# Optimization experiments

Hardware: AMD Instinct MI355X
Metric: run time of the kernel (lower is better)

The kernel has to match this reference:

```python
import jax, jax.numpy as jnp
import numpy as np
import math

B, S, H = 2, 2048, 4096
N_HEADS, HEAD_DIM = 32, 128
ROPE_THETA = 10000.0


def _rope_tables(seq_len, head_dim, dtype):
    inv_freq = 1.0 / (ROPE_THETA ** (jnp.arange(0, head_dim, 2, dtype=jnp.float32) / head_dim))
    t = jnp.arange(seq_len, dtype=jnp.float32)
    freqs = jnp.outer(t, inv_freq)                    # [S, D/2]
    emb = jnp.concatenate([freqs, freqs], axis=-1)    # [S, D]
    return jnp.cos(emb).astype(dtype), jnp.sin(emb).astype(dtype)


def _rotate_half(x):
    d = x.shape[-1] // 2
    return jnp.concatenate([-x[..., d:], x[..., :d]], axis=-1)


def setup_inputs() -> dict:
    key = jax.random.key(0)
    k0, k1, k2, k3, k4 = jax.random.split(key, 5)
    hidden_states = jax.random.normal(k0, (B, S, H), dtype=jnp.float32)
    # additive causal mask: 0 on/below diagonal, -1e9 above
    causal = jnp.triu(jnp.full((S, S), -1e9, dtype=jnp.float32), k=1)
    attention_mask = jnp.broadcast_to(causal, (B, 1, S, S))
    # BitNet b1.58 ternary weights {-1,0,1} with per-layer scalar scale
    wq = jax.random.randint(k1, (H, H), -1, 2).astype(jnp.float32)
    wk = jax.random.randint(k2, (H, H), -1, 2).astype(jnp.float32)
    wv = jax.random.randint(k3, (H, H), -1, 2).astype(jnp.float32)
    wo = jax.random.randint(k4, (H, H), -1, 2).astype(jnp.float32)
    scale = jnp.float32(0.02)
    return {"hidden_states": hidden_states, "attention_mask": attention_mask,
            "wq": wq, "wk": wk, "wv": wv, "wo": wo,
            "sq": scale, "sk": scale, "sv": scale, "so": scale}


def reference(hidden_states, attention_mask, wq, wk, wv, wo, sq, sk, sv, so):
    bsz, q_len, _ = hidden_states.shape
    dtype = hidden_states.dtype

    def qlin(x, w, s):  # QuantizedLinear: x @ (w_ternary * scale)^T
        return jnp.einsum('bsh,oh->bso', x, w) * s

    def split_heads(x):  # [B,S,H] -> [B,nH,S,D]
        return x.reshape(bsz, q_len, N_HEADS, HEAD_DIM).transpose(0, 2, 1, 3)

    q = split_heads(qlin(hidden_states, wq, sq))
    k = split_heads(qlin(hidden_states, wk, sk))
    v = split_heads(qlin(hidden_states, wv, sv))

    cos, sin = _rope_tables(q_len, HEAD_DIM, dtype)   # [S, D]
    q = q * cos + _rotate_half(q) * sin
    k = k * cos + _rotate_half(k) * sin

    scores = jnp.einsum('bnqd,bnkd->bnqk', q, k) / math.sqrt(HEAD_DIM)
    scores = scores + attention_mask
    scores = jnp.maximum(scores, jnp.finfo(scores.dtype).min)
    attn = jax.nn.softmax(scores, axis=-1)
    out = jnp.einsum('bnqk,bnkd->bnqd', attn, v)       # [B,nH,S,D]
    out = out.transpose(0, 2, 1, 3).reshape(bsz, q_len, N_HEADS * HEAD_DIM)
    return jnp.einsum('bsh,oh->bso', out, wo) * so
```

## Files before the change

### kernel.cpp

```cpp
#include <hip/hip_runtime.h>
#include <stdint.h>
#include <math.h>


#define HDIM   4096
#define SEQ    2048
#define NBATCH 2
#define NROWS  (NBATCH * SEQ)
#define NHEADS 32
#define DHEAD  128
#define QBLK   128

typedef __attribute__((ext_vector_type(8))) short short8;
typedef __attribute__((ext_vector_type(4))) short short4v;
typedef __attribute__((ext_vector_type(4))) float f32x4;
typedef unsigned short u16;
typedef unsigned int   u32;

__device__ __forceinline__ float bf2f(u16 u) {
  union { float f; u32 i; } x; x.i = ((u32)u) << 16; return x.f;
}
__device__ __forceinline__ u16 f2bf(float f) {
  union { float f; u32 i; } x; x.f = f;
  u32 r = x.i + 0x7FFFu + ((x.i >> 16) & 1u);
  return (u16)(r >> 16);
}
__device__ __forceinline__ u16 f2bf_t(float f) {
  union { float f; u32 i; } x; x.f = f;
  return (u16)(x.i >> 16);
}
__device__ __forceinline__ float exp2v(float x) {
  float r; asm("v_exp_f32 %0, %1" : "=v"(r) : "v"(x)); return r;
}

__device__ __forceinline__ void gload16(const u16* g, u16* l) {
  __builtin_amdgcn_global_load_lds(
      (const __attribute__((address_space(1))) u32*)g,
      (__attribute__((address_space(3))) u32*)l, 16, 0, 0);
}

__device__ __forceinline__ void unpack2(u32 v, float& a, float& b) {
  a = bf2f((u16)(v & 0xffffu)); b = bf2f((u16)(v >> 16));
}
__device__ __forceinline__ u32 pack2(float a, float b) {
  return (u32)f2bf(a) | ((u32)f2bf(b) << 16);
}

__global__ void f2bf_vec(const float* __restrict__ in, u16* __restrict__ out, int n4) {
  int i = blockIdx.x * blockDim.x + threadIdx.x;
  const int stride = gridDim.x * blockDim.x;
  for (; i < n4; i += stride) {
    float4 v = reinterpret_cast<const float4*>(in)[i];
    u32 lo = (u32)f2bf(v.x) | ((u32)f2bf(v.y) << 16);
    u32 hi = (u32)f2bf(v.z) | ((u32)f2bf(v.w) << 16);
    reinterpret_cast<uint2*>(out)[i] = make_uint2(lo, hi);
  }
}

__global__ void rope_tables_k(float* __restrict__ cosT, float* __restrict__ sinT) {
  int idx = blockIdx.x * blockDim.x + threadIdx.x;
  if (idx >= SEQ * 64) return;
  int s = idx >> 6, d = idx & 63;
  float ex = (float)(2 * d) / 128.0f;
  float inv = powf(10000.0f, -ex);
  float f = (float)s * inv;
  cosT[idx] = cosf(f);
  sinT[idx] = sinf(f);
}

template<int OUTF>
__global__ __launch_bounds__(512, 2)
void gemm8(const u16* __restrict__ Am, const u16* __restrict__ Bm,
           void* __restrict__ Cout, const float* __restrict__ scale_ptr,
           const float* __restrict__ cosT, const float* __restrict__ sinT) {
  extern __shared__ __align__(16) u16 ldsp[];

  const int tid = threadIdx.x;
  const int w = tid >> 6, lane = tid & 63;
  const int llo = lane & 15, lhi = (lane >> 4) & 3;
  const int wr = w >> 2, wc = w & 3;

  const int bid = blockIdx.x;
  const int xcd = bid & 7, ii = bid >> 3;
  const int by = (xcd >> 1) * 4 + (ii & 3);
  const int bx = (xcd & 1) * 8 + (ii >> 2);
  const int rowBase = by * 256, colBase = bx * 256;
  const float scl = scale_ptr[0];

  auto stage_half = [&](const u16* G, int obase, int ts, int h, int opB) {
    const int p = ts & 1;
    const u32 base = (opB ? 32768u : 0u) + (u32)p * 16384u + (u32)h * 8192u;
#pragma unroll
    for (int i = 0; i < 2; ++i) {
      const int ru = i * 64 + w * 8;
      const int r = ru + (lane >> 3);
      const int cc = (lane & 7) ^ (r & 7);
      gload16(G + (size_t)(obase + h * 128 + r) * HDIM + ts * 64 + cc * 8,
              ldsp + base + (u32)ru * 64u);
    }
  };

  f32x4 acc[8][4];
#pragma unroll
  for (int m = 0; m < 8; ++m)
#pragma unroll
    for (int n = 0; n < 4; ++n) acc[m][n] = (f32x4)0.0f;

#define PH(TCUR, MH, NH, TS, H, OPB, DOSTAGE, VMN) do {                          \
    const int p_ = (TCUR) & 1;                                                   \
    short8 af_[4][2]; short8 bf_[2][2];                                          \
    const u32 ab_ = (u32)(p_ * 16384 + (MH) * 8192);                             \
    const u32 bb_ = (u32)(32768 + p_ * 16384 + (NH) * 8192);                     \
    _Pragma("unroll")                                                            \
    for (int m4 = 0; m4 < 4; ++m4) { const int r_ = wr * 64 + m4 * 16 + llo;     \
      _Pragma("unroll")                                                          \
      for (int kk = 0; kk < 2; ++kk) { const int c_ = kk * 4 + lhi;              \
        af_[m4][kk] = *reinterpret_cast<const short8*>(                          \
            ldsp + ab_ + r_ * 64 + ((c_ ^ (r_ & 7)) * 8)); } }                   \
    _Pragma("unroll")                                                            \
    for (int n2 = 0; n2 < 2; ++n2) { const int r_ = wc * 32 + n2 * 16 + llo;     \
      _Pragma("unroll")                                                          \
      for (int kk = 0; kk < 2; ++kk) { const int c_ = kk * 4 + lhi;              \
        bf_[n2][kk] = *reinterpret_cast<const short8*>(                          \
            ldsp + bb_ + r_ * 64 + ((c_ ^ (r_ & 7)) * 8)); } }                   \
    if (DOSTAGE) stage_half((OPB) ? Bm : Am, (OPB) ? colBase : rowBase,          \
                            (TS), (H), (OPB));                                   \
    __builtin_amdgcn_s_barrier();                                                \
    asm volatile("s_waitcnt lgkmcnt(0)" ::: "memory");                           \
    __builtin_amdgcn_s_setprio(1);                                               \
    _Pragma("unroll")                                                            \
    for (int m4 = 0; m4 < 4; ++m4)                                               \
      _Pragma("unroll")                                                          \
      for (int n2 = 0; n2 < 2; ++n2)                                             \
        _Pragma("unroll")                                                        \
        for (int kk = 0; kk < 2; ++kk)                                           \
          acc[(MH) * 4 + m4][(NH) * 2 + n2] =                                    \
              __builtin_amdgcn_mfma_f32_16x16x32_bf16(                           \
                  af_[m4][kk], bf_[n2][kk],                                      \
                  acc[(MH) * 4 + m4][(NH) * 2 + n2], 0, 0, 0);                   \
    __builtin_amdgcn_s_setprio(0);                                               \
    if ((VMN) == 4) asm volatile("s_waitcnt vmcnt(4)" ::: "memory");             \
    if ((VMN) == 0) asm volatile("s_waitcnt vmcnt(0)" ::: "memory");             \
    __builtin_amdgcn_s_barrier();                                                \
  } while (0)

  stage_half(Am, rowBase, 0, 0, 0);
  stage_half(Bm, colBase, 0, 0, 1);
  stage_half(Am, rowBase, 0, 1, 0);
  stage_half(Bm, colBase, 0, 1, 1);
  stage_half(Am, rowBase, 1, 0, 0);
  stage_half(Bm, colBase, 1, 0, 1);
  asm volatile("s_waitcnt vmcnt(4)" ::: "memory");
  __builtin_amdgcn_s_barrier();

  for (int it = 0; it < 31; ++it) {
    const int T = 2 * it;
    PH(T,     0, 0, T + 1, 1, 0, 1, -1);
    PH(T,     0, 1, T + 1, 1, 1, 1, -1);
    PH(T,     1, 0, T + 2, 0, 0, 1, -1);
    PH(T,     1, 1, T + 2, 0, 1, 1,  4);
    PH(T + 1, 0, 0, T + 2, 1, 0, 1, -1);
    PH(T + 1, 0, 1, T + 2, 1, 1, 1, -1);
    PH(T + 1, 1, 0, T + 3, 0, 0, 1, -1);
    PH(T + 1, 1, 1, T + 3, 0, 1, 1,  4);
  }
  PH(62, 0, 0, 63, 1, 0, 1, -1);
  PH(62, 0, 1, 63, 1, 1, 1, -1);
  PH(62, 1, 0,  0, 0, 0, 0, -1);
  PH(62, 1, 1,  0, 0, 0, 0,  0);
  PH(63, 0, 0,  0, 0, 0, 0, -1);
  PH(63, 0, 1,  0, 0, 0, 0, -1);
  PH(63, 1, 0,  0, 0, 0, 0, -1);
  PH(63, 1, 1,  0, 0, 0, 0, -1);
#undef PH

  if (OUTF == 1) {
    float* ldf = reinterpret_cast<float*>(ldsp);
    float* Cf = reinterpret_cast<float*>(Cout);
#pragma unroll
    for (int hh = 0; hh < 2; ++hh) {
      if (hh) __syncthreads();
#pragma unroll
      for (int mf2 = 0; mf2 < 4; ++mf2)
#pragma unroll
        for (int nf = 0; nf < 4; ++nf)
#pragma unroll
          for (int r = 0; r < 4; ++r) {
            const int mf = hh * 4 + mf2;
            const int rowL = wr * 64 + mf2 * 16 + lhi * 4 + r;
            const int col = (nf >> 1) * 128 + wc * 32 + (nf & 1) * 16 + llo;
            ldf[rowL * 256 + col] = acc[mf][nf][r] * scl;
          }
      __syncthreads();
#pragma unroll
      for (int k = 0; k < 16; ++k) {
        const int rowL = k * 8 + w;
        const float4 v = *reinterpret_cast<const float4*>(&ldf[rowL * 256 + lane * 4]);
        *reinterpret_cast<float4*>(
            &Cf[(size_t)(rowBase + hh * 128 + rowL) * HDIM + colBase + lane * 4]) = v;
      }
    }
  } else {
#pragma unroll
    for (int mf = 0; mf < 8; ++mf)
#pragma unroll
      for (int nf = 0; nf < 4; ++nf)
#pragma unroll
        for (int r = 0; r < 4; ++r) {
          const int row = (mf >> 2) * 128 + wr * 64 + (mf & 3) * 16 + lhi * 4 + r;
          const int col = (nf >> 1) * 128 + wc * 32 + (nf & 1) * 16 + llo;
          ldsp[row * 256 + col] = f2bf(acc[mf][nf][r] * scl);
        }
    __syncthreads();
    u16* Cb = reinterpret_cast<u16*>(Cout);
#pragma unroll
    for (int k = 0; k < 16; ++k) {
      const int row = k * 16 + w * 2 + (lane >> 5);
      const int ch = lane & 31;
      if (OUTF == 2) {
        const int R = rowBase + row;
        const int pos = R & (SEQ - 1);
        const int cb = ch * 8;
        const int dl = cb & 63;
        const bool lohalf = (cb & 64) == 0;
        const short8 xv = *reinterpret_cast<const short8*>(&ldsp[row * 256 + cb]);
        const short8 pv = *reinterpret_cast<const short8*>(&ldsp[row * 256 + (cb ^ 64)]);
        const float* cT = &cosT[pos * 64 + dl];
        const float* sT = &sinT[pos * 64 + dl];
        u32 wds[4];
#pragma unroll
        for (int jj = 0; jj < 4; ++jj) {
          const float c0 = cT[jj * 2], c1 = cT[jj * 2 + 1];
          const float s0 = sT[jj * 2], s1 = sT[jj * 2 + 1];
          const float x0 = bf2f((u16)xv[jj * 2]), x1 = bf2f((u16)xv[jj * 2 + 1]);
          const float p0 = bf2f((u16)pv[jj * 2]), p1 = bf2f((u16)pv[jj * 2 + 1]);
          const float o0 = lohalf ? (x0 * c0 - p0 * s0) : (x0 * c0 + p0 * s0);
          const float o1 = lohalf ? (x1 * c1 - p1 * s1) : (x1 * c1 + p1 * s1);
          wds[jj] = pack2(o0, o1);
        }
        uint4 ov = make_uint4(wds[0], wds[1], wds[2], wds[3]);
        *reinterpret_cast<uint4*>(&Cb[(size_t)R * HDIM + colBase + cb]) = ov;
      } else {
        const short8 v = *reinterpret_cast<const short8*>(&ldsp[row * 256 + ch * 8]);
        *reinterpret_cast<short8*>(&Cb[(size_t)(rowBase + row) * HDIM + colBase + ch * 8]) = v;
      }
    }
  }
}

__global__ __launch_bounds__(512, 4)
void attn_causal(const u16* __restrict__ Q, const u16* __restrict__ K,
                 const u16* __restrict__ VT, u16* __restrict__ O) {
  __shared__ __align__(16) u16 Ks[2][64][128];
  __shared__ __align__(16) u16 Vt[128][72];
  __shared__ __align__(16) u16 Pw[8][16][76];

  const int tid = threadIdx.x;
  const int w = tid >> 6, lane = tid & 63;
  const int lhi = lane >> 4, llo = lane & 15;
  const int bh = blockIdx.y, b = bh >> 5, h = bh & 31;

  const u16* Kg = K + ((size_t)b * SEQ) * HDIM + h * DHEAD;
  const u16* VTg = VT + (size_t)(h * DHEAD) * NROWS + b * SEQ;

  const int kcp = tid & 15;
  const int vd = tid >> 2, vko = tid & 3;

  const float smul2 = 0.127517427f;
  int buf = 0;

  for (int halfq = 0; halfq < 2; ++halfq) {
    const int xq = (halfq == 0) ? (int)blockIdx.x : 15 - (int)blockIdx.x;
    const int qb = xq * QBLK;
    const int ntile = qb / 64 + 2;
    const int wmax = qb + w * 16 + 15;

    const u16* Qg = Q + ((size_t)(b * SEQ + qb)) * HDIM + h * DHEAD;
    short8 qf[4];
#pragma unroll
    for (int dc = 0; dc < 4; ++dc)
      qf[dc] = *reinterpret_cast<const short8*>(Qg + (size_t)(w * 16 + llo) * HDIM + dc * 32 + lhi * 8);

    f32x4 o[8];
#pragma unroll
    for (int dt = 0; dt < 8; ++dt) o[dt] = (f32x4)0.0f;
    float mrow[4], lrow[4];
#pragma unroll
    for (int r = 0; r < 4; ++r) { mrow[r] = -__builtin_inff(); lrow[r] = 0.0f; }

    {
      u16* dst = &Ks[buf][0][0] + tid * 8;
#pragma unroll
      for (int i = 0; i < 2; ++i) {
        const int r = i * 32 + (tid >> 4);
        const int cs = kcp ^ (r & 7);
        gload16(Kg + (size_t)r * HDIM + cs * 8, dst + i * 4096);
      }
    }
    short8 vreg0 = *reinterpret_cast<const short8*>(VTg + (size_t)vd * NROWS + vko * 8);
    short8 vreg1 = *reinterpret_cast<const short8*>(VTg + (size_t)vd * NROWS + 32 + vko * 8);

    for (int t = 0; t < ntile; ++t) {
      const int kv0 = t * 64;
      __syncthreads();
      *reinterpret_cast<short8*>(&Vt[vd][vko * 8]) = vreg0;
      *reinterpret_cast<short8*>(&Vt[vd][32 + vko * 8]) = vreg1;
      __syncthreads();
      if (t + 1 < ntile) {
        const int nkv = kv0 + 64;
        u16* dst = &Ks[buf ^ 1][0][0] + tid * 8;
#pragma unroll
        for (int i = 0; i < 2; ++i) {
          const int r = i * 32 + (tid >> 4);
          const int cs = kcp ^ (r & 7);
          gload16(Kg + (size_t)(nkv + r) * HDIM + cs * 8, dst + i * 4096);
        }
        vreg0 = *reinterpret_cast<const short8*>(VTg + (size_t)vd * NROWS + nkv + vko * 8);
        vreg1 = *reinterpret_cast<const short8*>(VTg + (size_t)vd * NROWS + nkv + 32 + vko * 8);
      }

      if (kv0 <= wmax) {
        f32x4 sacc[4];
#pragma unroll
        for (int nt2 = 0; nt2 < 4; ++nt2) sacc[nt2] = (f32x4)0.0f;
        __builtin_amdgcn_s_setprio(1);
#pragma unroll
        for (int nt2 = 0; nt2 < 4; ++nt2) {
          const int r = nt2 * 16 + llo;
#pragma unroll
          for (int dc = 0; dc < 4; ++dc) {
            const int cs = (dc * 4 + lhi) ^ (r & 7);
            const short8 kf = *reinterpret_cast<const short8*>(&Ks[buf][r][cs * 8]);
            sacc[nt2] = __builtin_amdgcn_mfma_f32_16x16x32_bf16(qf[dc], kf, sacc[nt2], 0, 0, 0);
          }
        }
        __builtin_amdgcn_s_setprio(0);

        float sv[4][4];
#pragma unroll
        for (int nt2 = 0; nt2 < 4; ++nt2)
#pragma unroll
          for (int r = 0; r < 4; ++r) {
            const int kcol = kv0 + nt2 * 16 + llo;
            const int qrow = qb + w * 16 + lhi * 4 + r;
            const float xv = sacc[nt2][r] * smul2;
            sv[nt2][r] = (kcol <= qrow) ? xv : -__builtin_inff();
          }

        float rmax[4];
#pragma unroll
        for (int r = 0; r < 4; ++r)
          rmax[r] = fmaxf(fmaxf(sv[0][r], sv[1][r]), fmaxf(sv[2][r], sv[3][r]));
#pragma unroll
        for (int xm = 1; xm < 16; xm <<= 1)
#pragma unroll
          for (int r = 0; r < 4; ++r) rmax[r] = fmaxf(rmax[r], __shfl_xor(rmax[r], xm));

        float p[4][4], fac[4], rsum[4];
#pragma unroll
        for (int r = 0; r < 4; ++r) {
          const float mn = fmaxf(mrow[r], rmax[r]);
          fac[r] = exp2v(mrow[r] - mn);
          mrow[r] = mn;
          p[0][r] = exp2v(sv[0][r] - mn);
          p[1][r] = exp2v(sv[1][r] - mn);
          p[2][r] = exp2v(sv[2][r] - mn);
          p[3][r] = exp2v(sv[3][r] - mn);
          rsum[r] = (p[0][r] + p[1][r]) + (p[2][r] + p[3][r]);
        }
#pragma unroll
        for (int xm = 1; xm < 16; xm <<= 1)
#pragma unroll
          for (int r = 0; r < 4; ++r) rsum[r] += __shfl_xor(rsum[r], xm);
#pragma unroll
        for (int r = 0; r < 4; ++r) lrow[r] = lrow[r] * fac[r] + rsum[r];
#pragma unroll
        for (int dt = 0; dt < 8; ++dt)
#pragma unroll
          for (int r = 0; r < 4; ++r) o[dt][r] *= fac[r];

#pragma unroll
        for (int nt2 = 0; nt2 < 4; ++nt2)
#pragma unroll
          for (int r = 0; r < 4; ++r)
            Pw[w][lhi * 4 + r][nt2 * 16 + llo] = f2bf_t(p[nt2][r]);

        union { short4v hh[2]; short8 v8; } pu[2];
#pragma unroll
        for (int s = 0; s < 2; ++s) {
          pu[s].hh[0] = *reinterpret_cast<const short4v*>(&Pw[w][llo][s * 32 + lhi * 8]);
          pu[s].hh[1] = *reinterpret_cast<const short4v*>(&Pw[w][llo][s * 32 + lhi * 8 + 4]);
        }
        __builtin_amdgcn_s_setprio(1);
#pragma unroll
        for (int dt = 0; dt < 8; ++dt)
#pragma unroll
          for (int s = 0; s < 2; ++s) {
            const short8 vf = *reinterpret_cast<const short8*>(&Vt[dt * 16 + llo][s * 32 + lhi * 8]);
            o[dt] = __builtin_amdgcn_mfma_f32_16x16x32_bf16(pu[s].v8, vf, o[dt], 0, 0, 0);
          }
        __builtin_amdgcn_s_setprio(0);
      }
      buf ^= 1;
    }

    u16* Og = O + ((size_t)(b * SEQ + qb)) * HDIM + h * DHEAD;
    float inv[4];
#pragma unroll
    for (int r = 0; r < 4; ++r) inv[r] = 1.0f / lrow[r];
#pragma unroll
    for (int dt = 0; dt < 8; ++dt)
#pragma unroll
      for (int r = 0; r < 4; ++r)
        Og[(size_t)(w * 16 + lhi * 4 + r) * HDIM + dt * 16 + llo] = f2bf(o[dt][r] * inv[r]);
  }
}

extern "C" void kernel_launch(void* const* d_in, const int* in_sizes, int n_in,
                              void* d_out, int out_size, void* d_ws, size_t ws_size,
                              hipStream_t stream) {
  (void)in_sizes; (void)n_in; (void)out_size; (void)ws_size;
  const float* hs = (const float*)d_in[0];
  const float* wq = (const float*)d_in[2];
  const float* wk = (const float*)d_in[3];
  const float* wv = (const float*)d_in[4];
  const float* wo = (const float*)d_in[5];
  const float* sq = (const float*)d_in[6];
  const float* sk = (const float*)d_in[7];
  const float* sv = (const float*)d_in[8];
  const float* so = (const float*)d_in[9];

  char* p = (char*)d_ws;
  const size_t MAT = (size_t)NROWS * HDIM * sizeof(u16);
  u16* Xb = (u16*)p; p += MAT;
  u16* Wb = (u16*)p; p += MAT;
  u16* Qb = (u16*)p; p += MAT;
  u16* Kb = (u16*)p; p += MAT;
  u16* Vb = (u16*)p; p += MAT;
  float* cosT = (float*)p; p += (size_t)SEQ * 64 * sizeof(float);
  float* sinT = (float*)p; p += (size_t)SEQ * 64 * sizeof(float);

  const int n4 = NROWS * (HDIM / 4);
  const dim3 cb(256);
  const int LDSZ = 131072;
  (void)hipFuncSetAttribute(reinterpret_cast<const void*>(&gemm8<0>),
                            hipFuncAttributeMaxDynamicSharedMemorySize, LDSZ);
  (void)hipFuncSetAttribute(reinterpret_cast<const void*>(&gemm8<1>),
                            hipFuncAttributeMaxDynamicSharedMemorySize, LDSZ);
  (void)hipFuncSetAttribute(reinterpret_cast<const void*>(&gemm8<2>),
                            hipFuncAttributeMaxDynamicSharedMemorySize, LDSZ);

  f2bf_vec<<<dim3(2048), cb, 0, stream>>>(hs, Xb, n4);
  rope_tables_k<<<dim3((SEQ * 64 + 255) / 256), cb, 0, stream>>>(cosT, sinT);

  f2bf_vec<<<dim3(2048), cb, 0, stream>>>(wq, Wb, n4);
  gemm8<2><<<dim3(256), dim3(512), LDSZ, stream>>>(Xb, Wb, (void*)Qb, sq, cosT, sinT);
  f2bf_vec<<<dim3(2048), cb, 0, stream>>>(wk, Wb, n4);
  gemm8<2><<<dim3(256), dim3(512), LDSZ, stream>>>(Xb, Wb, (void*)Kb, sk, cosT, sinT);
  f2bf_vec<<<dim3(2048), cb, 0, stream>>>(wv, Wb, n4);
  gemm8<0><<<dim3(256), dim3(512), LDSZ, stream>>>(Wb, Xb, (void*)Vb, sv, cosT, sinT);

  attn_causal<<<dim3(8, NBATCH * NHEADS), dim3(512), 0, stream>>>(Qb, Kb, Vb, Xb);

  f2bf_vec<<<dim3(2048), cb, 0, stream>>>(wo, Wb, n4);
  gemm8<1><<<dim3(256), dim3(512), LDSZ, stream>>>(Xb, Wb, d_out, so, cosT, sinT);
}
```

Measured before the change: 734.2 us.

## Stream V tiles via async direct-to-LDS loads and skip softmax rescale when max stable

V tiles are now fetched with direct global-to-LDS loads into a XOR-swizzled unpadded buffer, issued at the start of each iteration. An s_waitcnt/barrier sits between the QK/softmax phase and the PV MFMAs, so the V load overlaps score computation instead of passing through registers with two barriers. It also adds lazy online-softmax rescaling: o and l are only rescaled when some row's max grows by more than 8 (log2 units), which cuts the per-tile multiplies on the accumulators. This relies on the bounded-exponent tolerance of the lazy max and on correct vmcnt accounting for the K and V prefetches.

Measured after the change: 721.4 us. About the same (-1.8%).

```diff
diff --git a/kernel.cpp b/kernel.cpp
--- a/kernel.cpp
+++ b/kernel.cpp
@@ -252,7 +252,7 @@
 void attn_causal(const u16* __restrict__ Q, const u16* __restrict__ K,
                  const u16* __restrict__ VT, u16* __restrict__ O) {
   __shared__ __align__(16) u16 Ks[2][64][128];
-  __shared__ __align__(16) u16 Vt[128][72];
+  __shared__ __align__(16) u16 Vt[128][64];
   __shared__ __align__(16) u16 Pw[8][16][76];
 
   const int tid = threadIdx.x;
@@ -264,10 +264,9 @@
   const u16* VTg = VT + (size_t)(h * DHEAD) * NROWS + b * SEQ;
 
   const int kcp = tid & 15;
-  const int vd = tid >> 2, vko = tid & 3;
+  const int vrl = tid >> 3, vcp = tid & 7;
 
   const float smul2 = 0.127517427f;
-  int buf = 0;
 
   for (int halfq = 0; halfq < 2; ++halfq) {
     const int xq = (halfq == 0) ? (int)blockIdx.x : 15 - (int)blockIdx.x;
@@ -289,7 +288,7 @@
     for (int r = 0; r < 4; ++r) { mrow[r] = -__builtin_inff(); lrow[r] = 0.0f; }
 
     {
-      u16* dst = &Ks[buf][0][0] + tid * 8;
+      u16* dst = &Ks[0][0][0] + tid * 8;
 #pragma unroll
       for (int i = 0; i < 2; ++i) {
         const int r = i * 32 + (tid >> 4);
@@ -297,29 +296,35 @@
         gload16(Kg + (size_t)r * HDIM + cs * 8, dst + i * 4096);
       }
     }
-    short8 vreg0 = *reinterpret_cast<const short8*>(VTg + (size_t)vd * NROWS + vko * 8);
-    short8 vreg1 = *reinterpret_cast<const short8*>(VTg + (size_t)vd * NROWS + 32 + vko * 8);
+    __syncthreads();
+    int buf = 0;
 
     for (int t = 0; t < ntile; ++t) {
       const int kv0 = t * 64;
-      __syncthreads();
-      *reinterpret_cast<short8*>(&Vt[vd][vko * 8]) = vreg0;
-      *reinterpret_cast<short8*>(&Vt[vd][32 + vko * 8]) = vreg1;
-      __syncthreads();
-      if (t + 1 < ntile) {
+      {
+        u16* dst = &Vt[0][0] + tid * 8;
+#pragma unroll
+        for (int i = 0; i < 2; ++i) {
+          const int rV = i * 64 + vrl;
+          const int cs = vcp ^ (rV & 7);
+          gload16(VTg + (size_t)rV * NROWS + kv0 + cs * 8, dst + i * 4096);
+        }
+      }
+      const bool haveK = (t + 1 < ntile);
+      if (haveK) {
+        u16* dst = &Ks[buf ^ 1][0][0] + tid * 8;
         const int nkv = kv0 + 64;
-        u16* dst = &Ks[buf ^ 1][0][0] + tid * 8;
 #pragma unroll
         for (int i = 0; i < 2; ++i) {
           const int r = i * 32 + (tid >> 4);
           const int cs = kcp ^ (r & 7);
           gload16(Kg + (size_t)(nkv + r) * HDIM + cs * 8, dst + i * 4096);
         }
-        vreg0 = *reinterpret_cast<const short8*>(VTg + (size_t)vd * NROWS + nkv + vko * 8);
-        vreg1 = *reinterpret_cast<const short8*>(VTg + (size_t)vd * NROWS + nkv + 32 + vko * 8);
-      }
-
-      if (kv0 <= wmax) {
+      }
+
+      const bool docomp = (kv0 <= wmax);
+      union { short4v hh[2]; short8 v8; } pu[2];
+      if (docomp) {
         f32x4 sacc[4];
 #pragma unroll
         for (int nt2 = 0; nt2 < 4; ++nt2) sacc[nt2] = (f32x4)0.0f;
@@ -356,16 +361,32 @@
 #pragma unroll
           for (int r = 0; r < 4; ++r) rmax[r] = fmaxf(rmax[r], __shfl_xor(rmax[r], xm));
 
-        float p[4][4], fac[4], rsum[4];
+        bool need = false;
+#pragma unroll
+        for (int r = 0; r < 4; ++r) need = need || (rmax[r] > mrow[r] + 8.0f);
+        if (__any((int)need)) {
+          float fac[4];
+#pragma unroll
+          for (int r = 0; r < 4; ++r) {
+            const float mn = fmaxf(mrow[r], rmax[r]);
+            fac[r] = exp2v(mrow[r] - mn);
+            mrow[r] = mn;
+          }
+#pragma unroll
+          for (int r = 0; r < 4; ++r) lrow[r] *= fac[r];
+#pragma unroll
+          for (int dt = 0; dt < 8; ++dt)
+#pragma unroll
+            for (int r = 0; r < 4; ++r) o[dt][r] *= fac[r];
+        }
+
+        float p[4][4], rsum[4];
 #pragma unroll
         for (int r = 0; r < 4; ++r) {
-          const float mn = fmaxf(mrow[r], rmax[r]);
-          fac[r] = exp2v(mrow[r] - mn);
-          mrow[r] = mn;
-          p[0][r] = exp2v(sv[0][r] - mn);
-          p[1][r] = exp2v(sv[1][r] - mn);
-          p[2][r] = exp2v(sv[2][r] - mn);
-          p[3][r] = exp2v(sv[3][r] - mn);
+          p[0][r] = exp2v(sv[0][r] - mrow[r]);
+          p[1][r] = exp2v(sv[1][r] - mrow[r]);
+          p[2][r] = exp2v(sv[2][r] - mrow[r]);
+          p[3][r] = exp2v(sv[3][r] - mrow[r]);
           rsum[r] = (p[0][r] + p[1][r]) + (p[2][r] + p[3][r]);
         }
 #pragma unroll
@@ -373,11 +394,7 @@
 #pragma unroll
           for (int r = 0; r < 4; ++r) rsum[r] += __shfl_xor(rsum[r], xm);
 #pragma unroll
-        for (int r = 0; r < 4; ++r) lrow[r] = lrow[r] * fac[r] + rsum[r];
-#pragma unroll
-        for (int dt = 0; dt < 8; ++dt)
-#pragma unroll
-          for (int r = 0; r < 4; ++r) o[dt][r] *= fac[r];
+        for (int r = 0; r < 4; ++r) lrow[r] += rsum[r];
 
 #pragma unroll
         for (int nt2 = 0; nt2 < 4; ++nt2)
@@ -385,22 +402,31 @@
           for (int r = 0; r < 4; ++r)
             Pw[w][lhi * 4 + r][nt2 * 16 + llo] = f2bf_t(p[nt2][r]);
 
-        union { short4v hh[2]; short8 v8; } pu[2];
 #pragma unroll
         for (int s = 0; s < 2; ++s) {
           pu[s].hh[0] = *reinterpret_cast<const short4v*>(&Pw[w][llo][s * 32 + lhi * 8]);
           pu[s].hh[1] = *reinterpret_cast<const short4v*>(&Pw[w][llo][s * 32 + lhi * 8 + 4]);
         }
+      }
+
+      if (haveK) asm volatile("s_waitcnt vmcnt(2)" ::: "memory");
+      else       asm volatile("s_waitcnt vmcnt(0)" ::: "memory");
+      __builtin_amdgcn_s_barrier();
+
+      if (docomp) {
         __builtin_amdgcn_s_setprio(1);
 #pragma unroll
         for (int dt = 0; dt < 8; ++dt)
 #pragma unroll
           for (int s = 0; s < 2; ++s) {
-            const short8 vf = *reinterpret_cast<const short8*>(&Vt[dt * 16 + llo][s * 32 + lhi * 8]);
+            const int rr = dt * 16 + llo;
+            const int cs = (s * 4 + lhi) ^ (rr & 7);
+            const short8 vf = *reinterpret_cast<const short8*>(&Vt[rr][cs * 8]);
             o[dt] = __builtin_amdgcn_mfma_f32_16x16x32_bf16(pu[s].v8, vf, o[dt], 0, 0, 0);
           }
         __builtin_amdgcn_s_setprio(0);
       }
+      __syncthreads();
       buf ^= 1;
     }
 
```
